# Performance work log

Measured on AMD Instinct MI355X. Metric: run time of the kernel, lower is better.

The kernel has to match this reference:

```python
import jax, jax.numpy as jnp
import numpy as np

H = 16            # num_heads
DK = 64           # head_k_dim = hidden*0.5/H
DV = 128          # head_v_dim = hidden*1.0/H
EPS = 1e-5
GATE_NORM = 16.0


def setup_inputs() -> dict:
    key = jax.random.key(0)
    ks = jax.random.split(key, 8)
    B, T, D = 4, 4096, 2048
    hidden_states = jax.random.normal(ks[0], (B, T, D), jnp.float32)
    state = jax.random.normal(ks[1], (B, H, DK, DV), jnp.float32)
    norm_w = jnp.ones((D,), jnp.float32)
    # fan-in scaled init so activations stay O(1)
    k_w = jax.random.normal(ks[2], (H * DK, D), jnp.float32) / np.sqrt(D)
    v_w = jax.random.normal(ks[3], (H * DV, D), jnp.float32) / np.sqrt(D)
    gk_w1 = jax.random.normal(ks[4], (16, D), jnp.float32) / np.sqrt(D)
    gk_w2 = jax.random.normal(ks[5], (H * DK, 16), jnp.float32) / np.sqrt(16)
    gk_b = jnp.zeros((H * DK,), jnp.float32)
    return {"hidden_states": hidden_states, "state": state, "norm_w": norm_w,
            "k_w": k_w, "v_w": v_w, "gk_w1": gk_w1, "gk_w2": gk_w2, "gk_b": gk_b}


def reference(hidden_states, state, norm_w, k_w, v_w, gk_w1, gk_w2, gk_b):
    B, T, D = hidden_states.shape
    # RMSNorm
    x = hidden_states * jax.lax.rsqrt(jnp.mean(hidden_states * hidden_states, -1, keepdims=True) + EPS)
    x = x * norm_w
    # projections -> [B,T,H,d]
    k = (x @ k_w.T).reshape(B, T, H, DK)
    v = (x @ v_w.T).reshape(B, T, H, DV)
    gk = jax.nn.log_sigmoid((x @ gk_w1.T) @ gk_w2.T + gk_b) / GATE_NORM  # <= 0
    gk = gk.reshape(B, T, H, DK)
    # GLA recurrence S_t = diag(exp(gk_t)) S_{t-1} + k_t^T v_t, unrolled:
    # S_T = exp(G_T) * S_0 + sum_t exp(G_T - G_t) * k_t v_t^T, G_t = cumsum(gk)
    G = jnp.cumsum(gk, axis=1)                       # [B,T,H,DK]
    g_total = G[:, -1]                               # [B,H,DK]
    decay = jnp.exp(G[:, -1:, :, :] - G)             # in (0,1], stable
    new_state = jnp.exp(g_total)[..., None] * state + \
        jnp.einsum('bthk,bthv->bhkv', k * decay, v)
    return new_state
```

## Files before the change

kernel.cpp:

```cpp
#include <hip/hip_runtime.h>

#define B_ 4
#define T_ 4096
#define D_ 2048
#define H_ 16
#define DK_ 64
#define DV_ 128
#define HDK 1024
#define HDV 2048
#define NN 3072
#define MM 16384
#define KT_ 64

typedef unsigned short u16;
typedef unsigned int u32;
typedef __attribute__((ext_vector_type(8))) short bf16x8;
typedef __attribute__((ext_vector_type(4))) float f32x4;

typedef const __attribute__((address_space(1))) u16 gu16;
typedef __attribute__((address_space(3))) u16 lu16;

__device__ __forceinline__ float b2f(u16 u) {
  u32 x = ((u32)u) << 16; float f; __builtin_memcpy(&f, &x, 4); return f;
}
__device__ __forceinline__ u16 f2b(float f) {
  u32 x; __builtin_memcpy(&x, &f, 4);
  u32 r = x + 0x7FFFu + ((x >> 16) & 1u);
  return (u16)(r >> 16);
}
__device__ __forceinline__ float fexp(float x) { return exp2f(x * 1.44269504f); }
__device__ __forceinline__ float flogsig(float z) {
  float u = exp2f(-fabsf(z) * 1.44269504f);
  float l = log2f(1.f + u) * 0.69314718f;
  return fminf(z, 0.f) - l;
}

__global__ __launch_bounds__(256) void k_cvtw(const float* __restrict__ kw,
                                              const float* __restrict__ vw,
                                              u16* __restrict__ Wb) {
  int i = blockIdx.x * 256 + threadIdx.x;
  size_t e = (size_t)i * 8;
  const float* src = (e < (size_t)HDK * D_) ? (kw + e) : (vw + (e - (size_t)HDK * D_));
  float4 f0 = ((const float4*)src)[0];
  float4 f1 = ((const float4*)src)[1];
  union { int4 v; u16 u[8]; } o;
  o.u[0] = f2b(f0.x); o.u[1] = f2b(f0.y); o.u[2] = f2b(f0.z); o.u[3] = f2b(f0.w);
  o.u[4] = f2b(f1.x); o.u[5] = f2b(f1.y); o.u[6] = f2b(f1.z); o.u[7] = f2b(f1.w);
  *(int4*)(Wb + e) = o.v;
}

__global__ __launch_bounds__(256) void k_rms(const float* __restrict__ hs,
                                             const float* __restrict__ nw,
                                             const float* __restrict__ w1,
                                             u16* __restrict__ xb,
                                             float* __restrict__ y) {
  int r0 = blockIdx.x * 4;
  int tid = threadIdx.x;
  int wv = tid >> 6, ln = tid & 63;
  __shared__ float red[4][4];
  __shared__ float ys[4][4][16];
  float x[4][8];
  float ssq[4];
  #pragma unroll
  for (int r = 0; r < 4; ++r) {
    const float4* hp = (const float4*)(hs + (size_t)(r0 + r) * D_);
    float4 a = hp[tid * 2], b = hp[tid * 2 + 1];
    x[r][0] = a.x; x[r][1] = a.y; x[r][2] = a.z; x[r][3] = a.w;
    x[r][4] = b.x; x[r][5] = b.y; x[r][6] = b.z; x[r][7] = b.w;
    float s = 0.f;
    #pragma unroll
    for (int i = 0; i < 8; ++i) s += x[r][i] * x[r][i];
    #pragma unroll
    for (int o = 32; o > 0; o >>= 1) s += __shfl_xor(s, o, 64);
    ssq[r] = s;
  }
  if (ln == 0) {
    #pragma unroll
    for (int r = 0; r < 4; ++r) red[wv][r] = ssq[r];
  }
  __syncthreads();
  const float4* np_ = (const float4*)nw;
  float4 n0 = np_[tid * 2], n1 = np_[tid * 2 + 1];
  float nwv[8] = {n0.x, n0.y, n0.z, n0.w, n1.x, n1.y, n1.z, n1.w};
  #pragma unroll
  for (int r = 0; r < 4; ++r) {
    float tot = red[0][r] + red[1][r] + red[2][r] + red[3][r];
    float inv = rsqrtf(tot * (1.f / D_) + 1e-5f);
    union { int4 v; u16 u[8]; } o;
    #pragma unroll
    for (int i = 0; i < 8; ++i) { x[r][i] = x[r][i] * inv * nwv[i]; o.u[i] = f2b(x[r][i]); }
    *(int4*)(xb + (size_t)(r0 + r) * D_ + tid * 8) = o.v;
  }
  float p[4][16];
  #pragma unroll
  for (int r = 0; r < 4; ++r)
    #pragma unroll
    for (int j = 0; j < 16; ++j) p[r][j] = 0.f;
  #pragma unroll
  for (int j = 0; j < 16; ++j) {
    const float4* wp = (const float4*)(w1 + (size_t)j * D_);
    float4 a = wp[tid * 2], b = wp[tid * 2 + 1];
    float wj[8] = {a.x, a.y, a.z, a.w, b.x, b.y, b.z, b.w};
    #pragma unroll
    for (int r = 0; r < 4; ++r) {
      float s = 0.f;
      #pragma unroll
      for (int i = 0; i < 8; ++i) s += x[r][i] * wj[i];
      p[r][j] = s;
    }
  }
  #pragma unroll
  for (int r = 0; r < 4; ++r)
    #pragma unroll
    for (int j = 0; j < 16; ++j) {
      float s = p[r][j];
      #pragma unroll
      for (int o = 32; o > 0; o >>= 1) s += __shfl_xor(s, o, 64);
      p[r][j] = s;
    }
  if (ln == 0) {
    for (int r = 0; r < 4; ++r)
      for (int j = 0; j < 16; ++j) ys[wv][r][j] = p[r][j];
  }
  __syncthreads();
  if (tid < 64) {
    int r = tid >> 4, j = tid & 15;
    y[(size_t)(r0 + r) * 16 + j] = ys[0][r][j] + ys[1][r][j] + ys[2][r][j] + ys[3][r][j];
  }
}

#define STAGE4(GP, LB) do {                                                          \
    __builtin_amdgcn_global_load_lds((gu16*)(GP),             (lu16*)(LB),        16, 0, 0); \
    __builtin_amdgcn_global_load_lds((gu16*)((GP) + 16*2048), (lu16*)((LB)+512),  16, 0, 0); \
    __builtin_amdgcn_global_load_lds((gu16*)((GP) + 32*2048), (lu16*)((LB)+1024), 16, 0, 0); \
    __builtin_amdgcn_global_load_lds((gu16*)((GP) + 48*2048), (lu16*)((LB)+1536), 16, 0, 0); \
  } while (0)

#define GITER2(KTV, VMSTR, DO_STAGE) do {                                            \
    int slot_ = (KTV) & 3;                                                           \
    const u16* Ab_ = &SA[slot_][0];                                                  \
    const u16* Bb_ = &SB[slot_][0];                                                  \
                  \
    if (DO_STAGE) {                                                                  \
      const u16* gp_ = gsrc + (size_t)((KTV) + 3) * 32;                              \
      u16* lb_ = lbase + (((KTV) + 3) & 3) * 8192;                                   \
      __builtin_amdgcn_global_load_lds((gu16*)(gp_),             (lu16*)(lb_),       16, 0, 0); \
      __builtin_amdgcn_global_load_lds((gu16*)(gp_ + 16*2048),   (lu16*)(lb_+512),   16, 0, 0); \
    }                                                                                \
    bf16x8 bfr[4];                                                                   \
    _Pragma("unroll")                                                                \
    for (int ni = 0; ni < 4; ++ni)                                                   \
      bfr[ni] = *(const bf16x8*)(Bb_ + (wc * 64 + ni * 16 + r) * 32 + kcol);         \
    {                                                                                \
      bf16x8 a0 = *(const bf16x8*)(Ab_ + (wr * 128 + 0 * 16 + r) * 32 + kcol);       \
      bf16x8 a1 = *(const bf16x8*)(Ab_ + (wr * 128 + 1 * 16 + r) * 32 + kcol);       \
      bf16x8 a2 = *(const bf16x8*)(Ab_ + (wr * 128 + 2 * 16 + r) * 32 + kcol);       \
      bf16x8 a3 = *(const bf16x8*)(Ab_ + (wr * 128 + 3 * 16 + r) * 32 + kcol);       \
      __builtin_amdgcn_s_setprio(1);                                                 \
      _Pragma("unroll")                                                              \
      for (int ni = 0; ni < 4; ++ni) {                                               \
        acc[0][ni] = __builtin_amdgcn_mfma_f32_16x16x32_bf16(a0, bfr[ni], acc[0][ni], 0, 0, 0); \
        acc[1][ni] = __builtin_amdgcn_mfma_f32_16x16x32_bf16(a1, bfr[ni], acc[1][ni], 0, 0, 0); \
      }                                                                              \
      _Pragma("unroll")                                                              \
      for (int ni = 0; ni < 4; ++ni) {                                               \
        acc[2][ni] = __builtin_amdgcn_mfma_f32_16x16x32_bf16(a2, bfr[ni], acc[2][ni], 0, 0, 0); \
        acc[3][ni] = __builtin_amdgcn_mfma_f32_16x16x32_bf16(a3, bfr[ni], acc[3][ni], 0, 0, 0); \
      }                                                                              \
      __builtin_amdgcn_s_setprio(0);                                                 \
    }                                                                                \
    __builtin_amdgcn_s_barrier();                                                    \
    __builtin_amdgcn_sched_barrier(0);                                               \
                      \
    if (DO_STAGE) {                                                                  \
      const u16* gp_ = gsrc + (size_t)((KTV) + 3) * 32;                              \
      u16* lb_ = lbase + (((KTV) + 3) & 3) * 8192;                                   \
      __builtin_amdgcn_global_load_lds((gu16*)(gp_ + 32*2048),   (lu16*)(lb_+1024), 16, 0, 0); \
      __builtin_amdgcn_global_load_lds((gu16*)(gp_ + 48*2048),   (lu16*)(lb_+1536), 16, 0, 0); \
    }                                                                                \
    {                                                                                \
      bf16x8 a4 = *(const bf16x8*)(Ab_ + (wr * 128 + 4 * 16 + r) * 32 + kcol);       \
      bf16x8 a5 = *(const bf16x8*)(Ab_ + (wr * 128 + 5 * 16 + r) * 32 + kcol);       \
      bf16x8 a6 = *(const bf16x8*)(Ab_ + (wr * 128 + 6 * 16 + r) * 32 + kcol);       \
      bf16x8 a7 = *(const bf16x8*)(Ab_ + (wr * 128 + 7 * 16 + r) * 32 + kcol);       \
      __builtin_amdgcn_s_setprio(1);                                                 \
      _Pragma("unroll")                                                              \
      for (int ni = 0; ni < 4; ++ni) {                                               \
        acc[4][ni] = __builtin_amdgcn_mfma_f32_16x16x32_bf16(a4, bfr[ni], acc[4][ni], 0, 0, 0); \
        acc[5][ni] = __builtin_amdgcn_mfma_f32_16x16x32_bf16(a5, bfr[ni], acc[5][ni], 0, 0, 0); \
      }                                                                              \
      _Pragma("unroll")                                                              \
      for (int ni = 0; ni < 4; ++ni) {                                               \
        acc[6][ni] = __builtin_amdgcn_mfma_f32_16x16x32_bf16(a6, bfr[ni], acc[6][ni], 0, 0, 0); \
        acc[7][ni] = __builtin_amdgcn_mfma_f32_16x16x32_bf16(a7, bfr[ni], acc[7][ni], 0, 0, 0); \
      }                                                                              \
      __builtin_amdgcn_s_setprio(0);                                                 \
    }                                                                                \
    asm volatile("s_waitcnt vmcnt(" VMSTR ")" ::: "memory");                         \
    __builtin_amdgcn_s_barrier();                                                    \
    __builtin_amdgcn_sched_barrier(0);                                               \
  } while (0)

__global__ __launch_bounds__(512, 2) void k_gemm(const u16* __restrict__ X,
                                                 const u16* __restrict__ W,
                                                 u16* __restrict__ C) {
  __shared__ u16 SA[4][8192];
  __shared__ u16 SB[4][8192];
  int bid = blockIdx.x;
  int swzb = (bid & 7) * 96 + (bid >> 3);
  int tm = swzb / 12, tn = swzb - tm * 12;
  int m0 = tm << 8, n0 = tn << 8;
  int tid = threadIdx.x;
  int w = tid >> 6, l = tid & 63;
  int wr = w >> 2, wc = w & 3;
  int sw = w & 3;
  int srow = sw * 64 + (l >> 2);
  int cx = 8 * ((l & 3) ^ ((l >> 3) & 3));
  const u16* gsrc = ((w < 4) ? (X + (size_t)(m0 + srow) * D_)
                             : (W + (size_t)(n0 + srow) * D_)) + cx;
  u16* lbase = ((w < 4) ? &SA[0][0] : &SB[0][0]) + sw * 2048;
  int r = l & 15, kq = l >> 4;
  int kcol = (kq * 8) ^ (((r >> 1) & 3) << 3);

  f32x4 acc[8][4];
  #pragma unroll
  for (int mi = 0; mi < 8; ++mi)
    #pragma unroll
    for (int ni = 0; ni < 4; ++ni)
      #pragma unroll
      for (int q = 0; q < 4; ++q) acc[mi][ni][q] = 0.f;

  #pragma unroll
  for (int t = 0; t < 3; ++t) {
    const u16* gp_ = gsrc + (size_t)t * 32;
    u16* lb_ = lbase + t * 8192;
    STAGE4(gp_, lb_);
  }
  asm volatile("s_waitcnt vmcnt(8)" ::: "memory");
  __builtin_amdgcn_s_barrier();
  __builtin_amdgcn_sched_barrier(0);

  for (int kt = 0; kt < KT_ - 3; ++kt) GITER2(kt, "8", 1);
  GITER2(KT_ - 3, "4", 0);
  GITER2(KT_ - 2, "0", 0);
  GITER2(KT_ - 1, "0", 0);

  int cr = (l >> 4) * 4, cc = l & 15;
  #pragma unroll
  for (int mi = 0; mi < 8; ++mi)
    #pragma unroll
    for (int ni = 0; ni < 4; ++ni)
      #pragma unroll
      for (int q = 0; q < 4; ++q) {
        int gm = m0 + wr * 128 + mi * 16 + cr + q;
        int gn = n0 + wc * 64 + ni * 16 + cc;
        C[(size_t)gm * NN + gn] = f2b(acc[mi][ni][q]);
      }
}

__global__ __launch_bounds__(256) void k_gkcs(const float* __restrict__ y,
                                              const float* __restrict__ w2,
                                              const float* __restrict__ gb,
                                              u16* __restrict__ gkh,
                                              float* __restrict__ ct) {
  __shared__ float yl[64][16];
  int blk = blockIdx.x;
  int cg = blk & 3, tc = (blk >> 2) & 63, b = blk >> 8;
  int tid = threadIdx.x;
  int c = cg * 256 + tid;
  {
    int row = tid >> 2, q = tid & 3;
    const float4* src = (const float4*)(y + (size_t)(b * T_ + tc * 64 + row) * 16 + q * 4);
    *(float4*)&yl[row][q * 4] = *src;
  }
  float w2r[16];
  {
    const float4* wsrc = (const float4*)(w2 + (size_t)c * 16);
    float4 q0 = wsrc[0], q1 = wsrc[1], q2 = wsrc[2], q3 = wsrc[3];
    w2r[0] = q0.x; w2r[1] = q0.y; w2r[2] = q0.z; w2r[3] = q0.w;
    w2r[4] = q1.x; w2r[5] = q1.y; w2r[6] = q1.z; w2r[7] = q1.w;
    w2r[8] = q2.x; w2r[9] = q2.y; w2r[10] = q2.z; w2r[11] = q2.w;
    w2r[12] = q3.x; w2r[13] = q3.y; w2r[14] = q3.z; w2r[15] = q3.w;
  }
  float gbr = gb[c];
  __syncthreads();
  float sum = 0.f;
  size_t rowbase = (size_t)(b * T_ + tc * 64) * HDK + c;
  for (int t = 0; t < 64; ++t) {
    const float4* yv4 = (const float4*)&yl[t][0];
    float4 y0 = yv4[0], y1 = yv4[1], y2 = yv4[2], y3 = yv4[3];
    float z = gbr;
    z = fmaf(y0.x, w2r[0], z);  z = fmaf(y0.y, w2r[1], z);
    z = fmaf(y0.z, w2r[2], z);  z = fmaf(y0.w, w2r[3], z);
    z = fmaf(y1.x, w2r[4], z);  z = fmaf(y1.y, w2r[5], z);
    z = fmaf(y1.z, w2r[6], z);  z = fmaf(y1.w, w2r[7], z);
    z = fmaf(y2.x, w2r[8], z);  z = fmaf(y2.y, w2r[9], z);
    z = fmaf(y2.z, w2r[10], z); z = fmaf(y2.w, w2r[11], z);
    z = fmaf(y3.x, w2r[12], z); z = fmaf(y3.y, w2r[13], z);
    z = fmaf(y3.z, w2r[14], z); z = fmaf(y3.w, w2r[15], z);
    float g = flogsig(z) * (1.f / 16.f);
    _Float16 hv = (_Float16)g;
    u16 bits; __builtin_memcpy(&bits, &hv, 2);
    gkh[rowbase + (size_t)t * HDK] = bits;
    sum += (float)hv;
  }
  ct[(size_t)(b * 64 + tc) * HDK + c] = sum;
}

__global__ __launch_bounds__(256) void k_scan(const float* __restrict__ ct,
                                              float* __restrict__ co,
                                              float* __restrict__ gt) {
  int b = blockIdx.x >> 2, cg = blockIdx.x & 3;
  int c = cg * 256 + threadIdx.x;
  float run = 0.f;
  #pragma unroll 8
  for (int tc = 0; tc < 64; ++tc) {
    size_t idx = (size_t)(b * 64 + tc) * HDK + c;
    co[idx] = run;
    run += ct[idx];
  }
  gt[b * HDK + c] = run;
}

__global__ __launch_bounds__(256) void k_decay(const u16* __restrict__ gkh,
                                               const float* __restrict__ co,
                                               const float* __restrict__ gt,
                                               const u16* __restrict__ kv,
                                               u16* __restrict__ Ab) {
  int blk = blockIdx.x;
  int cg = blk & 3, tc = (blk >> 2) & 63, b = blk >> 8;
  int c = cg * 256 + threadIdx.x;
  float run = co[(size_t)(b * 64 + tc) * HDK + c];
  float g = gt[b * HDK + c];
  #pragma unroll 8
  for (int tt = 0; tt < 64; ++tt) {
    size_t row = (size_t)(b * T_) + tc * 64 + tt;
    u16 bits = gkh[row * HDK + c];
    _Float16 hv; __builtin_memcpy(&hv, &bits, 2);
    run += (float)hv;
    float decay = fexp(g - run);
    float kvl = b2f(kv[row * NN + c]);
    Ab[row * HDK + c] = f2b(kvl * decay);
  }
}

__global__ __launch_bounds__(256) void k_outer(const u16* __restrict__ Ab,
                                               const u16* __restrict__ kv,
                                               float* __restrict__ part) {
  __shared__ u16 At[2][64][40];
  __shared__ u16 Vt[2][128][40];
  int s = blockIdx.x, h = blockIdx.y, b = blockIdx.z;
  int tid = threadIdx.x;
  int w = tid >> 6, l = tid & 63;
  int adk = tid & 63, atq = tid >> 6;
  int vdv = tid & 127, vth = tid >> 7;
  int r = l & 15, q = l >> 4;
  f32x4 acc[8];
  #pragma unroll
  for (int n = 0; n < 8; ++n)
    #pragma unroll
    for (int j = 0; j < 4; ++j) acc[n][j] = 0.f;

  union { int4 v[2]; u16 u[16]; } vbuf;
  union { int4 v; u16 u[8]; } abuf;

  #define LOADT(KK) do {                                                              \
      int t0_ = s * 256 + (KK) * 32;                                                  \
      _Pragma("unroll")                                                               \
      for (int i = 0; i < 8; ++i)                                                     \
        abuf.u[i] = Ab[(size_t)(b * T_ + t0_ + atq * 8 + i) * HDK + h * DK_ + adk];   \
      _Pragma("unroll")                                                               \
      for (int i = 0; i < 16; ++i)                                                    \
        vbuf.u[i] = kv[(size_t)(b * T_ + t0_ + vth * 16 + i) * NN + HDK + h * DV_ + vdv]; \
    } while (0)

  #define WRITET(BF) do {                                                             \
      *(int4*)&At[BF][adk][atq * 8] = abuf.v;                                         \
      *(int4*)&Vt[BF][vdv][vth * 16] = vbuf.v[0];                                     \
      *(int4*)&Vt[BF][vdv][vth * 16 + 8] = vbuf.v[1];                                 \
    } while (0)

  LOADT(0);
  WRITET(0);
  for (int kk = 0; kk < 8; ++kk) {
    int cur = kk & 1;
    if (kk < 7) LOADT(kk + 1);
    __syncthreads();
    bf16x8 af = *(const bf16x8*)&At[cur][w * 16 + r][q * 8];
    #pragma unroll
    for (int n = 0; n < 8; ++n) {
      bf16x8 vf = *(const bf16x8*)&Vt[cur][n * 16 + r][q * 8];
      acc[n] = __builtin_amdgcn_mfma_f32_16x16x32_bf16(af, vf, acc[n], 0, 0, 0);
    }
    __syncthreads();
    if (kk < 7) WRITET(1 - cur);
  }
  #undef LOADT
  #undef WRITET

  float* dst = part + ((size_t)(b * H_ + h) * 16 + s) * (DK_ * DV_);
  #pragma unroll
  for (int n = 0; n < 8; ++n)
    #pragma unroll
    for (int j = 0; j < 4; ++j)
      dst[(w * 16 + q * 4 + j) * DV_ + n * 16 + r] = acc[n][j];
}

__global__ __launch_bounds__(256) void k_final(const float* __restrict__ part,
                                               const float* __restrict__ gt,
                                               const float* __restrict__ st,
                                               float* __restrict__ out) {
  int i = blockIdx.x * 256 + threadIdx.x;
  int dv = i & 127, dk = (i >> 7) & 63, h = (i >> 13) & 15, b = i >> 17;
  size_t base = ((size_t)(b * H_ + h) * 16) * 8192 + dk * DV_ + dv;
  float s = 0.f;
  #pragma unroll
  for (int sp = 0; sp < 16; ++sp) s += part[base + (size_t)sp * 8192];
  float g = gt[b * HDK + h * DK_ + dk];
  out[i] = fexp(g) * st[i] + s;
}

extern "C" void kernel_launch(void* const* d_in, const int* in_sizes, int n_in,
                              void* d_out, int out_size, void* d_ws, size_t ws_size,
                              hipStream_t stream) {
  const float* hs = (const float*)d_in[0];
  const float* st = (const float*)d_in[1];
  const float* nw = (const float*)d_in[2];
  const float* kw = (const float*)d_in[3];
  const float* vw = (const float*)d_in[4];
  const float* w1 = (const float*)d_in[5];
  const float* w2 = (const float*)d_in[6];
  const float* gb = (const float*)d_in[7];
  float* out = (float*)d_out;
  char* ws = (char*)d_ws;

  u16*  Wb  = (u16*)(ws + 0);
  u16*  xb  = (u16*)(ws + 12582912);
  float* y  = (float*)(ws + 79691776);
  u16*  kv  = (u16*)(ws + 80740352);
  u16*  gkh = (u16*)(ws + 181403648);
  float* ct = (float*)(ws + 214958080);
  float* co = (float*)(ws + 216006656);
  float* gt = (float*)(ws + 217055232);
  u16*  Ab  = (u16*)(ws + 12582912);
  float* part = (float*)(ws + 12582912 + 33554432);

  k_cvtw<<<dim3(3072), dim3(256), 0, stream>>>(kw, vw, Wb);
  k_rms<<<dim3(4096), dim3(256), 0, stream>>>(hs, nw, w1, xb, y);
  k_gemm<<<dim3(768), dim3(512), 0, stream>>>(xb, Wb, kv);
  k_gkcs<<<dim3(1024), dim3(256), 0, stream>>>(y, w2, gb, gkh, ct);
  k_scan<<<dim3(16), dim3(256), 0, stream>>>(ct, co, gt);
  k_decay<<<dim3(1024), dim3(256), 0, stream>>>(gkh, co, gt, kv, Ab);
  k_outer<<<dim3(16, 16, 4), dim3(256), 0, stream>>>(Ab, kv, part);
  k_final<<<dim3(2048), dim3(256), 0, stream>>>(part, gt, st, out);
}
```

Baseline: 375.7 us.

## Restructure GEMM main loop into double-buffered 64-wide k tiles split into halves

Replaces the 4-slot ring buffer (32-wide k steps, prefetch three ahead, two barriers per step) with a double buffer of 64-wide k tiles, each consumed in two 32-wide half steps. Every wave now stages part of both A and B instead of splitting waves between X and W loaders. Each half step waits, synchronises once, then loads all 8 A fragments and runs 32 MFMAs. The aim is to halve the barrier count and simplify the pipeline. In exchange the prefetch distance becomes shorter, so load latency is hidden less, and holding all A fragments at once raises register pressure.

```diff
diff --git a/kernel.cpp b/kernel.cpp
--- a/kernel.cpp
+++ b/kernel.cpp
@@ -10,7 +10,7 @@
 #define HDV 2048
 #define NN 3072
 #define MM 16384
-#define KT_ 64
+#define NT_ 32
 
 typedef unsigned short u16;
 typedef unsigned int u32;
@@ -129,83 +129,42 @@
   }
 }
 
-#define STAGE4(GP, LB) do {                                                          \
-    __builtin_amdgcn_global_load_lds((gu16*)(GP),             (lu16*)(LB),        16, 0, 0); \
-    __builtin_amdgcn_global_load_lds((gu16*)((GP) + 16*2048), (lu16*)((LB)+512),  16, 0, 0); \
-    __builtin_amdgcn_global_load_lds((gu16*)((GP) + 32*2048), (lu16*)((LB)+1024), 16, 0, 0); \
-    __builtin_amdgcn_global_load_lds((gu16*)((GP) + 48*2048), (lu16*)((LB)+1536), 16, 0, 0); \
-  } while (0)
-
-#define GITER2(KTV, VMSTR, DO_STAGE) do {                                            \
-    int slot_ = (KTV) & 3;                                                           \
-    const u16* Ab_ = &SA[slot_][0];                                                  \
-    const u16* Bb_ = &SB[slot_][0];                                                  \
-                  \
-    if (DO_STAGE) {                                                                  \
-      const u16* gp_ = gsrc + (size_t)((KTV) + 3) * 32;                              \
-      u16* lb_ = lbase + (((KTV) + 3) & 3) * 8192;                                   \
-      __builtin_amdgcn_global_load_lds((gu16*)(gp_),             (lu16*)(lb_),       16, 0, 0); \
-      __builtin_amdgcn_global_load_lds((gu16*)(gp_ + 16*2048),   (lu16*)(lb_+512),   16, 0, 0); \
-    }                                                                                \
-    bf16x8 bfr[4];                                                                   \
-    _Pragma("unroll")                                                                \
-    for (int ni = 0; ni < 4; ++ni)                                                   \
-      bfr[ni] = *(const bf16x8*)(Bb_ + (wc * 64 + ni * 16 + r) * 32 + kcol);         \
-    {                                                                                \
-      bf16x8 a0 = *(const bf16x8*)(Ab_ + (wr * 128 + 0 * 16 + r) * 32 + kcol);       \
-      bf16x8 a1 = *(const bf16x8*)(Ab_ + (wr * 128 + 1 * 16 + r) * 32 + kcol);       \
-      bf16x8 a2 = *(const bf16x8*)(Ab_ + (wr * 128 + 2 * 16 + r) * 32 + kcol);       \
-      bf16x8 a3 = *(const bf16x8*)(Ab_ + (wr * 128 + 3 * 16 + r) * 32 + kcol);       \
-      __builtin_amdgcn_s_setprio(1);                                                 \
-      _Pragma("unroll")                                                              \
-      for (int ni = 0; ni < 4; ++ni) {                                               \
-        acc[0][ni] = __builtin_amdgcn_mfma_f32_16x16x32_bf16(a0, bfr[ni], acc[0][ni], 0, 0, 0); \
-        acc[1][ni] = __builtin_amdgcn_mfma_f32_16x16x32_bf16(a1, bfr[ni], acc[1][ni], 0, 0, 0); \
-      }                                                                              \
-      _Pragma("unroll")                                                              \
-      for (int ni = 0; ni < 4; ++ni) {                                               \
-        acc[2][ni] = __builtin_amdgcn_mfma_f32_16x16x32_bf16(a2, bfr[ni], acc[2][ni], 0, 0, 0); \
-        acc[3][ni] = __builtin_amdgcn_mfma_f32_16x16x32_bf16(a3, bfr[ni], acc[3][ni], 0, 0, 0); \
-      }                                                                              \
-      __builtin_amdgcn_s_setprio(0);                                                 \
-    }                                                                                \
-    __builtin_amdgcn_s_barrier();                                                    \
-    __builtin_amdgcn_sched_barrier(0);                                               \
-                      \
-    if (DO_STAGE) {                                                                  \
-      const u16* gp_ = gsrc + (size_t)((KTV) + 3) * 32;                              \
-      u16* lb_ = lbase + (((KTV) + 3) & 3) * 8192;                                   \
-      __builtin_amdgcn_global_load_lds((gu16*)(gp_ + 32*2048),   (lu16*)(lb_+1024), 16, 0, 0); \
-      __builtin_amdgcn_global_load_lds((gu16*)(gp_ + 48*2048),   (lu16*)(lb_+1536), 16, 0, 0); \
-    }                                                                                \
-    {                                                                                \
-      bf16x8 a4 = *(const bf16x8*)(Ab_ + (wr * 128 + 4 * 16 + r) * 32 + kcol);       \
-      bf16x8 a5 = *(const bf16x8*)(Ab_ + (wr * 128 + 5 * 16 + r) * 32 + kcol);       \
-      bf16x8 a6 = *(const bf16x8*)(Ab_ + (wr * 128 + 6 * 16 + r) * 32 + kcol);       \
-      bf16x8 a7 = *(const bf16x8*)(Ab_ + (wr * 128 + 7 * 16 + r) * 32 + kcol);       \
-      __builtin_amdgcn_s_setprio(1);                                                 \
-      _Pragma("unroll")                                                              \
-      for (int ni = 0; ni < 4; ++ni) {                                               \
-        acc[4][ni] = __builtin_amdgcn_mfma_f32_16x16x32_bf16(a4, bfr[ni], acc[4][ni], 0, 0, 0); \
-        acc[5][ni] = __builtin_amdgcn_mfma_f32_16x16x32_bf16(a5, bfr[ni], acc[5][ni], 0, 0, 0); \
-      }                                                                              \
-      _Pragma("unroll")                                                              \
-      for (int ni = 0; ni < 4; ++ni) {                                               \
-        acc[6][ni] = __builtin_amdgcn_mfma_f32_16x16x32_bf16(a6, bfr[ni], acc[6][ni], 0, 0, 0); \
-        acc[7][ni] = __builtin_amdgcn_mfma_f32_16x16x32_bf16(a7, bfr[ni], acc[7][ni], 0, 0, 0); \
-      }                                                                              \
-      __builtin_amdgcn_s_setprio(0);                                                 \
-    }                                                                                \
-    asm volatile("s_waitcnt vmcnt(" VMSTR ")" ::: "memory");                         \
-    __builtin_amdgcn_s_barrier();                                                    \
-    __builtin_amdgcn_sched_barrier(0);                                               \
+#define GLDS(SRC, DST) __builtin_amdgcn_global_load_lds((gu16*)(SRC), (lu16*)(DST), 16, 0, 0)
+
+#define HALFSTEP(DB, KH, NB, KTN, VMSTR, DO_STAGE) do {                        \
+    if (DO_STAGE) {                                                            \
+      const u16* a_ = Ag + (size_t)(KTN) * 64 + (KH) * 32;                     \
+      const u16* b_ = Bg + (size_t)(KTN) * 64 + (KH) * 32;                     \
+      GLDS(a_,            &SA[NB][KH][lw]);                                    \
+      GLDS(a_ + 16 * D_,  &SA[NB][KH][lw + 512]);                              \
+      GLDS(b_,            &SB[NB][KH][lw]);                                    \
+      GLDS(b_ + 16 * D_,  &SB[NB][KH][lw + 512]);                              \
+    }                                                                          \
+    asm volatile("s_waitcnt vmcnt(" VMSTR ")" ::: "memory");                   \
+    __builtin_amdgcn_s_barrier();                                              \
+    __builtin_amdgcn_sched_barrier(0);                                         \
+    bf16x8 bfr[4];                                                             \
+    _Pragma("unroll")                                                          \
+    for (int ni = 0; ni < 4; ++ni)                                             \
+      bfr[ni] = *(const bf16x8*)&SB[DB][KH][(wc * 64 + ni * 16 + r) * 32 + kcol]; \
+    bf16x8 afr[8];                                                             \
+    _Pragma("unroll")                                                          \
+    for (int mi = 0; mi < 8; ++mi)                                             \
+      afr[mi] = *(const bf16x8*)&SA[DB][KH][(wr * 128 + mi * 16 + r) * 32 + kcol]; \
+    __builtin_amdgcn_s_setprio(1);                                             \
+    _Pragma("unroll")                                                          \
+    for (int mi = 0; mi < 8; ++mi)                                             \
+      _Pragma("unroll")                                                        \
+      for (int ni = 0; ni < 4; ++ni)                                           \
+        acc[mi][ni] = __builtin_amdgcn_mfma_f32_16x16x32_bf16(afr[mi], bfr[ni], acc[mi][ni], 0, 0, 0); \
+    __builtin_amdgcn_s_setprio(0);                                             \
   } while (0)
 
 __global__ __launch_bounds__(512, 2) void k_gemm(const u16* __restrict__ X,
                                                  const u16* __restrict__ W,
                                                  u16* __restrict__ C) {
-  __shared__ u16 SA[4][8192];
-  __shared__ u16 SB[4][8192];
+  __shared__ u16 SA[2][2][8192];
+  __shared__ u16 SB[2][2][8192];
   int bid = blockIdx.x;
   int swzb = (bid & 7) * 96 + (bid >> 3);
   int tm = swzb / 12, tn = swzb - tm * 12;
@@ -213,14 +172,13 @@
   int tid = threadIdx.x;
   int w = tid >> 6, l = tid & 63;
   int wr = w >> 2, wc = w & 3;
-  int sw = w & 3;
-  int srow = sw * 64 + (l >> 2);
-  int cx = 8 * ((l & 3) ^ ((l >> 3) & 3));
-  const u16* gsrc = ((w < 4) ? (X + (size_t)(m0 + srow) * D_)
-                             : (W + (size_t)(n0 + srow) * D_)) + cx;
-  u16* lbase = ((w < 4) ? &SA[0][0] : &SB[0][0]) + sw * 2048;
+  int arow = w * 32 + (l >> 2);
+  int csw = 8 * ((l & 3) ^ ((l >> 3) & 3));
+  const u16* Ag = X + (size_t)(m0 + arow) * D_ + csw;
+  const u16* Bg = W + (size_t)(n0 + arow) * D_ + csw;
+  int lw = w * 1024;
   int r = l & 15, kq = l >> 4;
-  int kcol = (kq * 8) ^ (((r >> 1) & 3) << 3);
+  int kcol = 8 * (kq ^ ((r >> 1) & 3));
 
   f32x4 acc[8][4];
   #pragma unroll
@@ -231,19 +189,20 @@
       for (int q = 0; q < 4; ++q) acc[mi][ni][q] = 0.f;
 
   #pragma unroll
-  for (int t = 0; t < 3; ++t) {
-    const u16* gp_ = gsrc + (size_t)t * 32;
-    u16* lb_ = lbase + t * 8192;
-    STAGE4(gp_, lb_);
-  }
-  asm volatile("s_waitcnt vmcnt(8)" ::: "memory");
-  __builtin_amdgcn_s_barrier();
-  __builtin_amdgcn_sched_barrier(0);
-
-  for (int kt = 0; kt < KT_ - 3; ++kt) GITER2(kt, "8", 1);
-  GITER2(KT_ - 3, "4", 0);
-  GITER2(KT_ - 2, "0", 0);
-  GITER2(KT_ - 1, "0", 0);
+  for (int kh = 0; kh < 2; ++kh) {
+    GLDS(Ag + kh * 32,           &SA[0][kh][lw]);
+    GLDS(Ag + kh * 32 + 16 * D_, &SA[0][kh][lw + 512]);
+    GLDS(Bg + kh * 32,           &SB[0][kh][lw]);
+    GLDS(Bg + kh * 32 + 16 * D_, &SB[0][kh][lw + 512]);
+  }
+
+  for (int kt = 0; kt < NT_ - 1; ++kt) {
+    int db = kt & 1, nb = db ^ 1;
+    HALFSTEP(db, 0, nb, kt + 1, "8", 1);
+    HALFSTEP(db, 1, nb, kt + 1, "8", 1);
+  }
+  HALFSTEP(1, 0, 0, 0, "4", 0);
+  HALFSTEP(1, 1, 0, 0, "0", 0);
 
   int cr = (l >> 4) * 4, cc = l & 15;
   #pragma unroll
```

Result: no change. 369.6 us (-1.6%).
